# Optimization experiments

Hardware: AMD Instinct MI355X
Metric: run time of the kernel (lower is better)

## Reference

```python
import jax, jax.numpy as jnp
import numpy as np

VOCAB = 50000
D = 300          # w2v vector_size
B = 2048         # sentences
L = 64           # maxlen
S = 2048         # total seeds (= sum of num_clusters[0])
C = 64           # clusters
LS = 8           # maxlen_seed
ANPHA = 0.5


def setup_inputs() -> dict:
    key = jax.random.key(0)
    ks = jax.random.split(key, 4)
    return {
        "sents": jax.random.randint(ks[0], (B, L), 0, VOCAB),
        "seeds": jax.random.randint(ks[1], (S, LS), 0, VOCAB),
        "num_clusters": jnp.full((1, C), S // C, dtype=jnp.int32),
        "num_arr": 0,
        "mask": jnp.ones((B, L), jnp.float32),
        "flag": 1,
        "emb_teacher": jax.random.normal(ks[2], (VOCAB, D), jnp.float32) * 0.1,
        "emb_student": jax.random.normal(ks[3], (VOCAB, D), jnp.float32) * 0.1,
    }


def _sent_emb(tok_emb, mask):
    # masked mean pooling over tokens: tok_emb [B,L,D], mask [B,L]
    denom = jnp.clip(mask.sum(-1, keepdims=True), 1.0)
    return (tok_emb * mask[..., None]).sum(1) / denom


def _seed_emb(tok_emb):
    # plain mean pooling over seed-phrase tokens: [S,LS,D] -> [S,D]
    return tok_emb.mean(1)


def _segment_max_arg(pro, lens):
    # pro [B,S]; lens [C] segment lengths summing to S (ragged segments along axis 1)
    Ssz = pro.shape[1]
    Csz = lens.shape[0]
    csum = jnp.cumsum(lens)
    starts = csum - lens
    seg = jnp.searchsorted(csum, jnp.arange(Ssz), side="right")   # [S] segment ids
    m = jax.ops.segment_max(pro.T, seg, num_segments=Csz)          # [C,B] per-segment max
    is_max = pro.T == m[seg]                                       # [S,B]
    local = jnp.arange(Ssz) - starts[seg]                          # index within segment
    arg = jax.ops.segment_min(jnp.where(is_max, local[:, None], Ssz), seg,
                              num_segments=Csz)                    # first argmax (torch tie rule)
    return m.T, arg.T                                              # [B,C], [B,C]


def _normalize(x):
    # Normalize(): class-probabilities + reliability (confidence vs uniform)
    p = jax.nn.softmax(x, axis=-1)
    reli = jnp.max(p, axis=-1, keepdims=True) - 1.0 / x.shape[-1]
    return p, reli


def reference(sents, seeds, num_clusters, num_arr, mask, flag,
              emb_teacher, emb_student):
    lens = num_clusters[0]

    # teacher branch
    snt_t = _sent_emb(emb_teacher[sents], mask)        # [B,D]
    sd_t = _seed_emb(emb_teacher[seeds])               # [S,D]
    pro_t = jnp.einsum("bd,sd->bs", snt_t, sd_t)       # [B,S]

    # student branch
    snt_s = _sent_emb(emb_student[sents], mask)
    sd_s = _seed_emb(emb_student[seeds])
    pro_s = jnp.einsum("bd,sd->bs", snt_s, sd_s)

    # ragged per-cluster max / argmax (replaces the torch loop + cat)
    pro_s_max, index_max = _segment_max_arg(pro_s, lens)   # [B,C]
    pro_t_max, _ = _segment_max_arg(pro_t, lens)           # [B,C]

    predict_t, reli_t = _normalize(pro_t_max)

    if flag:  # flag is a static python int -> loss branch
        denta = predict_t - pro_s_max
        loss = ((1.0 + ANPHA * jnp.abs(reli_t)) * denta * denta).sum()
        return loss / predict_t.shape[0]
    else:
        return jnp.argmax(pro_s_max, axis=-1)
```

## Files before the change

### kernel.cpp

```cpp
#include <hip/hip_runtime.h>
#include <hip/hip_bf16.h>

#define BB 2048
#define LL 64
#define SS 2048
#define LSEED 8
#define CC 64
#define DD 300
#define KP 320
#define TPAD 48

typedef __attribute__((ext_vector_type(8))) short short8;
typedef __attribute__((ext_vector_type(4))) float f32x4;

__device__ __forceinline__ unsigned enc_f(float f) {
    unsigned u = __float_as_uint(f);
    return (u & 0x80000000u) ? ~u : (u | 0x80000000u);
}
__device__ __forceinline__ float dec_f(unsigned k) {
    unsigned u = (k & 0x80000000u) ? (k ^ 0x80000000u) : ~k;
    return __uint_as_float(u);
}

__global__ void init_kernel(const int* __restrict__ lens,
                            unsigned* __restrict__ keys ,
                            int* __restrict__ seg ) {
    int i = blockIdx.x * 256 + threadIdx.x;
    if (i < 2 * BB * CC) keys[i] = 0u;
    if (i < SS) {
        int c = 0, cum = lens[0];
        while (i >= cum && c < CC - 1) { c++; cum += lens[c]; }
        seg[i] = c;
    }
}

__global__ __launch_bounds__(320) void pool_kernel(
    const int* __restrict__ sents, const int* __restrict__ seeds,
    const float* __restrict__ mask,
    const float* __restrict__ emb_t, const float* __restrict__ emb_s,
    __hip_bfloat16* __restrict__ snt_t, __hip_bfloat16* __restrict__ snt_s,
    __hip_bfloat16* __restrict__ sd_t, __hip_bfloat16* __restrict__ sd_s) {
    int bid = blockIdx.x, tid = threadIdx.x;
    __shared__ int toks[LL];
    __shared__ float msk[LL];
    __shared__ float denom_sh;
    if (bid < BB) {
        int b = bid;
        if (tid < LL) {
            float v = mask[b * LL + tid];
            msk[tid] = v;
            toks[tid] = sents[b * LL + tid];
#pragma unroll
            for (int d = 32; d; d >>= 1) v += __shfl_xor(v, d);
            if (tid == 0) denom_sh = fmaxf(v, 1.0f);
        }
        __syncthreads();
        float at = 0.f, as = 0.f;
        if (tid < DD) {
#pragma unroll 4
            for (int l = 0; l < LL; l++) {
                long o = (long)toks[l] * DD + tid;
                float m = msk[l];
                at = fmaf(m, emb_t[o], at);
                as = fmaf(m, emb_s[o], as);
            }
        }
        float inv = 1.0f / denom_sh;
        float vt = (tid < DD) ? at * inv : 0.f;
        float vs = (tid < DD) ? as * inv : 0.f;
        snt_t[(size_t)b * KP + tid] = __float2bfloat16(vt);
        snt_s[(size_t)b * KP + tid] = __float2bfloat16(vs);
    } else {
        int s = bid - BB;
        if (tid < LSEED) toks[tid] = seeds[s * LSEED + tid];
        __syncthreads();
        float at = 0.f, as = 0.f;
        if (tid < DD) {
#pragma unroll
            for (int l = 0; l < LSEED; l++) {
                long o = (long)toks[l] * DD + tid;
                at += emb_t[o];
                as += emb_s[o];
            }
        }
        float vt = (tid < DD) ? at * (1.0f / LSEED) : 0.f;
        float vs = (tid < DD) ? as * (1.0f / LSEED) : 0.f;
        sd_t[(size_t)s * KP + tid] = __float2bfloat16(vt);
        sd_s[(size_t)s * KP + tid] = __float2bfloat16(vs);
    }
}

__global__ __launch_bounds__(256) void gemm_max_kernel(
    const __hip_bfloat16* __restrict__ snt_t, const __hip_bfloat16* __restrict__ snt_s,
    const __hip_bfloat16* __restrict__ sd_t, const __hip_bfloat16* __restrict__ sd_s,
    const int* __restrict__ seg,
    unsigned* __restrict__ keys_t, unsigned* __restrict__ keys_s) {
    const int branch = blockIdx.z;
    const __hip_bfloat16* Ag = branch ? snt_s : snt_t;
    const __hip_bfloat16* Bg = branch ? sd_s : sd_t;
    unsigned* keys = branch ? keys_s : keys_t;

    const int tid = threadIdx.x;
    const int wave = tid >> 6, lane = tid & 63;
    const int quad = lane >> 4, l16 = lane & 15;
    const int wm = wave >> 1, wn = wave & 1;
    const int row0 = blockIdx.y * 128, col0 = blockIdx.x * 128;

    __shared__ __align__(16) char smem[33792 + 512];
    __hip_bfloat16* As = (__hip_bfloat16*)smem;
    __hip_bfloat16* Bs = As + 128 * TPAD;
    float* Dl = (float*)smem;
    int* segs = (int*)(smem + 33792);

    if (tid < 128) segs[tid] = seg[col0 + tid];

    f32x4 acc[4][4];
#pragma unroll
    for (int i = 0; i < 4; i++)
#pragma unroll
        for (int j = 0; j < 4; j++) acc[i][j] = (f32x4)0.f;

    for (int kt = 0; kt < KP / 32; kt++) {
        const int k0 = kt * 32;
        __syncthreads();
#pragma unroll
        for (int i = 0; i < 2; i++) {
            int c = tid + 256 * i;
            int r = c >> 2, p = c & 3;
            *(float4*)(As + r * TPAD + p * 8) =
                *(const float4*)(Ag + (size_t)(row0 + r) * KP + k0 + p * 8);
            *(float4*)(Bs + r * TPAD + p * 8) =
                *(const float4*)(Bg + (size_t)(col0 + r) * KP + k0 + p * 8);
        }
        __syncthreads();
        short8 af[4], bfr[4];
#pragma unroll
        for (int mt = 0; mt < 4; mt++)
            af[mt] = *(const short8*)(As + (wm * 64 + mt * 16 + l16) * TPAD + quad * 8);
#pragma unroll
        for (int nt = 0; nt < 4; nt++)
            bfr[nt] = *(const short8*)(Bs + (wn * 64 + nt * 16 + l16) * TPAD + quad * 8);
#pragma unroll
        for (int mt = 0; mt < 4; mt++)
#pragma unroll
            for (int nt = 0; nt < 4; nt++)
                acc[mt][nt] = __builtin_amdgcn_mfma_f32_16x16x32_bf16(
                    af[mt], bfr[nt], acc[mt][nt], 0, 0, 0);
    }

#pragma unroll 1
    for (int h = 0; h < 2; h++) {
        __syncthreads();
        if (wn == h) {
#pragma unroll
            for (int mt = 0; mt < 4; mt++)
#pragma unroll
                for (int nt = 0; nt < 4; nt++)
#pragma unroll
                    for (int reg = 0; reg < 4; reg++)
                        Dl[(wm * 64 + mt * 16 + quad * 4 + reg) * 66 + nt * 16 + l16] =
                            acc[mt][nt][reg];
        }
        __syncthreads();
        int r = tid >> 1, j0 = (tid & 1) * 32;
        float cur = Dl[r * 66 + j0];
        int cs = segs[h * 64 + j0];
#pragma unroll
        for (int j = 1; j < 32; j++) {
            int sgj = segs[h * 64 + j0 + j];
            float v = Dl[r * 66 + j0 + j];
            if (sgj == cs) {
                cur = fmaxf(cur, v);
            } else {
                atomicMax(&keys[(size_t)(row0 + r) * CC + cs], enc_f(cur));
                cs = sgj;
                cur = v;
            }
        }
        atomicMax(&keys[(size_t)(row0 + r) * CC + cs], enc_f(cur));
    }
}

__global__ __launch_bounds__(256) void loss_kernel(
    const unsigned* __restrict__ keys_t, const unsigned* __restrict__ keys_s,
    float* __restrict__ partials) {
    int tid = threadIdx.x, w = tid >> 6, lane = tid & 63;
    int row = blockIdx.x * 4 + w;
    float t = dec_f(keys_t[row * CC + lane]);
    float s = dec_f(keys_s[row * CC + lane]);
    float m = t;
#pragma unroll
    for (int d = 32; d; d >>= 1) m = fmaxf(m, __shfl_xor(m, d));
    float e = expf(t - m);
    float sum = e;
#pragma unroll
    for (int d = 32; d; d >>= 1) sum += __shfl_xor(sum, d);
    float p = e / sum;
    float reli = 1.0f / sum - (1.0f / CC);
    float denta = p - s;
    float term = (1.0f + 0.5f * fabsf(reli)) * denta * denta;
#pragma unroll
    for (int d = 32; d; d >>= 1) term += __shfl_xor(term, d);
    __shared__ float blk[4];
    if (lane == 0) blk[w] = term;
    __syncthreads();
    if (tid == 0) partials[blockIdx.x] = blk[0] + blk[1] + blk[2] + blk[3];
}

__global__ void final_kernel(const float* __restrict__ partials, float* __restrict__ out) {
    int tid = threadIdx.x;
    float v = partials[tid] + partials[tid + 256];
#pragma unroll
    for (int d = 32; d; d >>= 1) v += __shfl_xor(v, d);
    __shared__ float blk[4];
    if ((tid & 63) == 0) blk[tid >> 6] = v;
    __syncthreads();
    if (tid == 0) out[0] = (blk[0] + blk[1] + blk[2] + blk[3]) * (1.0f / BB);
}

extern "C" void kernel_launch(void* const* d_in, const int* in_sizes, int n_in,
                              void* d_out, int out_size, void* d_ws, size_t ws_size,
                              hipStream_t stream) {
    const int*   sents = (const int*)d_in[0];
    const int*   seeds = (const int*)d_in[1];
    const int*   lens  = (const int*)d_in[2];
    const float* mask  = (const float*)d_in[4];
    const float* emb_t = (const float*)d_in[6];
    const float* emb_s = (const float*)d_in[7];
    float* out = (float*)d_out;

    char* w = (char*)d_ws;
    __hip_bfloat16* snt_t = (__hip_bfloat16*)w; w += (size_t)BB * KP * 2;
    __hip_bfloat16* snt_s = (__hip_bfloat16*)w; w += (size_t)BB * KP * 2;
    __hip_bfloat16* sd_t  = (__hip_bfloat16*)w; w += (size_t)SS * KP * 2;
    __hip_bfloat16* sd_s  = (__hip_bfloat16*)w; w += (size_t)SS * KP * 2;
    unsigned* keys_t = (unsigned*)w; w += (size_t)BB * CC * 4;
    unsigned* keys_s = (unsigned*)w; w += (size_t)BB * CC * 4;
    int* seg = (int*)w;              w += (size_t)SS * 4;
    float* partials = (float*)w;     w += (size_t)(BB / 4) * 4;

    init_kernel<<<(2 * BB * CC + 255) / 256, 256, 0, stream>>>(lens, keys_t, seg);
    pool_kernel<<<BB + SS, 320, 0, stream>>>(sents, seeds, mask, emb_t, emb_s,
                                             snt_t, snt_s, sd_t, sd_s);
    gemm_max_kernel<<<dim3(SS / 128, BB / 128, 2), 256, 0, stream>>>(
        snt_t, snt_s, sd_t, sd_s, seg, keys_t, keys_s);
    loss_kernel<<<BB / 4, 256, 0, stream>>>(keys_t, keys_s, partials);
    final_kernel<<<1, 256, 0, stream>>>(partials, out);
}
```

Baseline: 198.8 us.

## Fuse init into pooling, vectorize gathers, use direct-to-LDS loads, atomic final sum

Folds the key/segment initialization into the pooling kernel and replaces the final reduction kernel with an atomicAdd in the loss kernel, cutting two launches. Pooling now uses 256 threads that each gather float4 chunks, with three token groups reduced through shared memory. The GEMM tile loads use global_load_lds to write straight into unpadded LDS instead of going through registers, which may add LDS bank conflicts on the fragment reads. Keys are zeroed by pool blocks, which works only because BB+SS blocks times 64 equals 2*BB*CC, and the float atomicAdd makes the final sum order nondeterministic.

```diff
diff --git a/kernel.cpp b/kernel.cpp
--- a/kernel.cpp
+++ b/kernel.cpp
@@ -7,8 +7,8 @@
 #define LSEED 8
 #define CC 64
 #define DD 300
+#define NC4 75
 #define KP 320
-#define TPAD 48
 
 typedef __attribute__((ext_vector_type(8))) short short8;
 typedef __attribute__((ext_vector_type(4))) float f32x4;
@@ -21,31 +21,48 @@
     unsigned u = (k & 0x80000000u) ? (k ^ 0x80000000u) : ~k;
     return __uint_as_float(u);
 }
-
-__global__ void init_kernel(const int* __restrict__ lens,
-                            unsigned* __restrict__ keys ,
-                            int* __restrict__ seg ) {
-    int i = blockIdx.x * 256 + threadIdx.x;
-    if (i < 2 * BB * CC) keys[i] = 0u;
-    if (i < SS) {
-        int c = 0, cum = lens[0];
-        while (i >= cum && c < CC - 1) { c++; cum += lens[c]; }
-        seg[i] = c;
-    }
-}
-
-__global__ __launch_bounds__(320) void pool_kernel(
+__device__ __forceinline__ unsigned short f2bf(float f) {
+    unsigned u = __float_as_uint(f);
+    u += 0x7fffu + ((u >> 16) & 1u);
+    return (unsigned short)(u >> 16);
+}
+__device__ __forceinline__ void gload_lds16(const void* g, void* l) {
+    __builtin_amdgcn_global_load_lds(
+        (const __attribute__((address_space(1))) void*)g,
+        (__attribute__((address_space(3))) void*)l, 16, 0, 0);
+}
+
+__global__ __launch_bounds__(256) void pool_kernel(
     const int* __restrict__ sents, const int* __restrict__ seeds,
-    const float* __restrict__ mask,
+    const int* __restrict__ lens, const float* __restrict__ mask,
     const float* __restrict__ emb_t, const float* __restrict__ emb_s,
-    __hip_bfloat16* __restrict__ snt_t, __hip_bfloat16* __restrict__ snt_s,
-    __hip_bfloat16* __restrict__ sd_t, __hip_bfloat16* __restrict__ sd_s) {
-    int bid = blockIdx.x, tid = threadIdx.x;
+    unsigned short* __restrict__ snt_t, unsigned short* __restrict__ snt_s,
+    unsigned short* __restrict__ sd_t, unsigned short* __restrict__ sd_s,
+    unsigned* __restrict__ keys_all, int* __restrict__ seg,
+    float* __restrict__ out0) {
+    const int bid = blockIdx.x, tid = threadIdx.x;
+
+    if (tid < 64) keys_all[bid * 64 + tid] = 0u;
+    if (bid == 0) {
+        if (tid == 0) *out0 = 0.f;
+        for (int i = tid * 8; i < tid * 8 + 8; i++) {
+            int c = 0, cum = lens[0];
+            while (i >= cum && c < CC - 1) { c++; cum += lens[c]; }
+            seg[i] = c;
+        }
+    }
+
+    __shared__ float4 pt[3 * NC4];
+    __shared__ float4 ps[3 * NC4];
     __shared__ int toks[LL];
     __shared__ float msk[LL];
     __shared__ float denom_sh;
+
+    const int g = tid / NC4;
+    const int c = tid - g * NC4;
+
     if (bid < BB) {
-        int b = bid;
+        const int b = bid;
         if (tid < LL) {
             float v = mask[b * LL + tid];
             msk[tid] = v;
@@ -55,49 +72,86 @@
             if (tid == 0) denom_sh = fmaxf(v, 1.0f);
         }
         __syncthreads();
-        float at = 0.f, as = 0.f;
-        if (tid < DD) {
+        if (g < 3) {
+            float4 at = {0.f, 0.f, 0.f, 0.f}, as = {0.f, 0.f, 0.f, 0.f};
 #pragma unroll 4
-            for (int l = 0; l < LL; l++) {
-                long o = (long)toks[l] * DD + tid;
+            for (int l = g; l < LL; l += 3) {
+                size_t o = (size_t)toks[l] * DD;
                 float m = msk[l];
-                at = fmaf(m, emb_t[o], at);
-                as = fmaf(m, emb_s[o], as);
+                float4 vt = *(const float4*)(emb_t + o + 4 * c);
+                float4 vs = *(const float4*)(emb_s + o + 4 * c);
+                at.x = fmaf(m, vt.x, at.x); at.y = fmaf(m, vt.y, at.y);
+                at.z = fmaf(m, vt.z, at.z); at.w = fmaf(m, vt.w, at.w);
+                as.x = fmaf(m, vs.x, as.x); as.y = fmaf(m, vs.y, as.y);
+                as.z = fmaf(m, vs.z, as.z); as.w = fmaf(m, vs.w, as.w);
             }
-        }
-        float inv = 1.0f / denom_sh;
-        float vt = (tid < DD) ? at * inv : 0.f;
-        float vs = (tid < DD) ? as * inv : 0.f;
-        snt_t[(size_t)b * KP + tid] = __float2bfloat16(vt);
-        snt_s[(size_t)b * KP + tid] = __float2bfloat16(vs);
+            pt[g * NC4 + c] = at;
+            ps[g * NC4 + c] = as;
+        }
+        __syncthreads();
+        float scale = 1.0f / denom_sh;
+        if (tid < 150) {
+            int table = tid / NC4, cc = tid - table * NC4;
+            const float4* P = table ? ps : pt;
+            float4 a = P[cc], b2 = P[NC4 + cc], d2 = P[2 * NC4 + cc];
+            ushort4 o;
+            o.x = f2bf((a.x + b2.x + d2.x) * scale);
+            o.y = f2bf((a.y + b2.y + d2.y) * scale);
+            o.z = f2bf((a.z + b2.z + d2.z) * scale);
+            o.w = f2bf((a.w + b2.w + d2.w) * scale);
+            unsigned short* dst = (table ? snt_s : snt_t) + (size_t)b * KP + 4 * cc;
+            *(ushort4*)dst = o;
+        } else if (tid >= 160 && tid < 170) {
+            int k = tid - 160;
+            unsigned short* dst = ((k < 5) ? snt_t : snt_s) + (size_t)b * KP + 300 + 4 * (k % 5);
+            *(ushort4*)dst = (ushort4){0, 0, 0, 0};
+        }
     } else {
-        int s = bid - BB;
+        const int s = bid - BB;
         if (tid < LSEED) toks[tid] = seeds[s * LSEED + tid];
         __syncthreads();
-        float at = 0.f, as = 0.f;
-        if (tid < DD) {
-#pragma unroll
-            for (int l = 0; l < LSEED; l++) {
-                long o = (long)toks[l] * DD + tid;
-                at += emb_t[o];
-                as += emb_s[o];
+        if (g < 3) {
+            float4 at = {0.f, 0.f, 0.f, 0.f}, as = {0.f, 0.f, 0.f, 0.f};
+#pragma unroll
+            for (int l = g; l < LSEED; l += 3) {
+                size_t o = (size_t)toks[l] * DD;
+                float4 vt = *(const float4*)(emb_t + o + 4 * c);
+                float4 vs = *(const float4*)(emb_s + o + 4 * c);
+                at.x += vt.x; at.y += vt.y; at.z += vt.z; at.w += vt.w;
+                as.x += vs.x; as.y += vs.y; as.z += vs.z; as.w += vs.w;
             }
-        }
-        float vt = (tid < DD) ? at * (1.0f / LSEED) : 0.f;
-        float vs = (tid < DD) ? as * (1.0f / LSEED) : 0.f;
-        sd_t[(size_t)s * KP + tid] = __float2bfloat16(vt);
-        sd_s[(size_t)s * KP + tid] = __float2bfloat16(vs);
+            pt[g * NC4 + c] = at;
+            ps[g * NC4 + c] = as;
+        }
+        __syncthreads();
+        const float scale = 1.0f / LSEED;
+        if (tid < 150) {
+            int table = tid / NC4, cc = tid - table * NC4;
+            const float4* P = table ? ps : pt;
+            float4 a = P[cc], b2 = P[NC4 + cc], d2 = P[2 * NC4 + cc];
+            ushort4 o;
+            o.x = f2bf((a.x + b2.x + d2.x) * scale);
+            o.y = f2bf((a.y + b2.y + d2.y) * scale);
+            o.z = f2bf((a.z + b2.z + d2.z) * scale);
+            o.w = f2bf((a.w + b2.w + d2.w) * scale);
+            unsigned short* dst = (table ? sd_s : sd_t) + (size_t)s * KP + 4 * cc;
+            *(ushort4*)dst = o;
+        } else if (tid >= 160 && tid < 170) {
+            int k = tid - 160;
+            unsigned short* dst = ((k < 5) ? sd_t : sd_s) + (size_t)s * KP + 300 + 4 * (k % 5);
+            *(ushort4*)dst = (ushort4){0, 0, 0, 0};
+        }
     }
 }
 
 __global__ __launch_bounds__(256) void gemm_max_kernel(
-    const __hip_bfloat16* __restrict__ snt_t, const __hip_bfloat16* __restrict__ snt_s,
-    const __hip_bfloat16* __restrict__ sd_t, const __hip_bfloat16* __restrict__ sd_s,
+    const unsigned short* __restrict__ snt_t, const unsigned short* __restrict__ snt_s,
+    const unsigned short* __restrict__ sd_t, const unsigned short* __restrict__ sd_s,
     const int* __restrict__ seg,
     unsigned* __restrict__ keys_t, unsigned* __restrict__ keys_s) {
     const int branch = blockIdx.z;
-    const __hip_bfloat16* Ag = branch ? snt_s : snt_t;
-    const __hip_bfloat16* Bg = branch ? sd_s : sd_t;
+    const unsigned short* Ag = branch ? snt_s : snt_t;
+    const unsigned short* Bg = branch ? sd_s : sd_t;
     unsigned* keys = branch ? keys_s : keys_t;
 
     const int tid = threadIdx.x;
@@ -107,39 +161,41 @@
     const int row0 = blockIdx.y * 128, col0 = blockIdx.x * 128;
 
     __shared__ __align__(16) char smem[33792 + 512];
-    __hip_bfloat16* As = (__hip_bfloat16*)smem;
-    __hip_bfloat16* Bs = As + 128 * TPAD;
+    unsigned short* As = (unsigned short*)smem;
+    unsigned short* Bs = As + 128 * 32;
     float* Dl = (float*)smem;
     int* segs = (int*)(smem + 33792);
 
     if (tid < 128) segs[tid] = seg[col0 + tid];
 
+    const int lr = lane >> 2, lp = lane & 3;
+
     f32x4 acc[4][4];
 #pragma unroll
     for (int i = 0; i < 4; i++)
 #pragma unroll
         for (int j = 0; j < 4; j++) acc[i][j] = (f32x4)0.f;
 
+#pragma unroll 1
     for (int kt = 0; kt < KP / 32; kt++) {
         const int k0 = kt * 32;
         __syncthreads();
 #pragma unroll
         for (int i = 0; i < 2; i++) {
-            int c = tid + 256 * i;
-            int r = c >> 2, p = c & 3;
-            *(float4*)(As + r * TPAD + p * 8) =
-                *(const float4*)(Ag + (size_t)(row0 + r) * KP + k0 + p * 8);
-            *(float4*)(Bs + r * TPAD + p * 8) =
-                *(const float4*)(Bg + (size_t)(col0 + r) * KP + k0 + p * 8);
+            int rb = wave * 32 + i * 16;
+            gload_lds16(Ag + (size_t)(row0 + rb + lr) * KP + k0 + lp * 8,
+                        As + rb * 32);
+            gload_lds16(Bg + (size_t)(col0 + rb + lr) * KP + k0 + lp * 8,
+                        Bs + rb * 32);
         }
         __syncthreads();
         short8 af[4], bfr[4];
 #pragma unroll
         for (int mt = 0; mt < 4; mt++)
-            af[mt] = *(const short8*)(As + (wm * 64 + mt * 16 + l16) * TPAD + quad * 8);
+            af[mt] = *(const short8*)(As + (wm * 64 + mt * 16 + l16) * 32 + quad * 8);
 #pragma unroll
         for (int nt = 0; nt < 4; nt++)
-            bfr[nt] = *(const short8*)(Bs + (wn * 64 + nt * 16 + l16) * TPAD + quad * 8);
+            bfr[nt] = *(const short8*)(Bs + (wn * 64 + nt * 16 + l16) * 32 + quad * 8);
 #pragma unroll
         for (int mt = 0; mt < 4; mt++)
 #pragma unroll
@@ -183,7 +239,7 @@
 
 __global__ __launch_bounds__(256) void loss_kernel(
     const unsigned* __restrict__ keys_t, const unsigned* __restrict__ keys_s,
-    float* __restrict__ partials) {
+    float* __restrict__ out) {
     int tid = threadIdx.x, w = tid >> 6, lane = tid & 63;
     int row = blockIdx.x * 4 + w;
     float t = dec_f(keys_t[row * CC + lane]);
@@ -204,18 +260,8 @@
     __shared__ float blk[4];
     if (lane == 0) blk[w] = term;
     __syncthreads();
-    if (tid == 0) partials[blockIdx.x] = blk[0] + blk[1] + blk[2] + blk[3];
-}
-
-__global__ void final_kernel(const float* __restrict__ partials, float* __restrict__ out) {
-    int tid = threadIdx.x;
-    float v = partials[tid] + partials[tid + 256];
-#pragma unroll
-    for (int d = 32; d; d >>= 1) v += __shfl_xor(v, d);
-    __shared__ float blk[4];
-    if ((tid & 63) == 0) blk[tid >> 6] = v;
-    __syncthreads();
-    if (tid == 0) out[0] = (blk[0] + blk[1] + blk[2] + blk[3]) * (1.0f / BB);
+    if (tid == 0)
+        atomicAdd(out, (blk[0] + blk[1] + blk[2] + blk[3]) * (1.0f / BB));
 }
 
 extern "C" void kernel_launch(void* const* d_in, const int* in_sizes, int n_in,
@@ -230,20 +276,18 @@
     float* out = (float*)d_out;
 
     char* w = (char*)d_ws;
-    __hip_bfloat16* snt_t = (__hip_bfloat16*)w; w += (size_t)BB * KP * 2;
-    __hip_bfloat16* snt_s = (__hip_bfloat16*)w; w += (size_t)BB * KP * 2;
-    __hip_bfloat16* sd_t  = (__hip_bfloat16*)w; w += (size_t)SS * KP * 2;
-    __hip_bfloat16* sd_s  = (__hip_bfloat16*)w; w += (size_t)SS * KP * 2;
+    unsigned short* snt_t = (unsigned short*)w; w += (size_t)BB * KP * 2;
+    unsigned short* snt_s = (unsigned short*)w; w += (size_t)BB * KP * 2;
+    unsigned short* sd_t  = (unsigned short*)w; w += (size_t)SS * KP * 2;
+    unsigned short* sd_s  = (unsigned short*)w; w += (size_t)SS * KP * 2;
     unsigned* keys_t = (unsigned*)w; w += (size_t)BB * CC * 4;
     unsigned* keys_s = (unsigned*)w; w += (size_t)BB * CC * 4;
     int* seg = (int*)w;              w += (size_t)SS * 4;
-    float* partials = (float*)w;     w += (size_t)(BB / 4) * 4;
-
-    init_kernel<<<(2 * BB * CC + 255) / 256, 256, 0, stream>>>(lens, keys_t, seg);
-    pool_kernel<<<BB + SS, 320, 0, stream>>>(sents, seeds, mask, emb_t, emb_s,
-                                             snt_t, snt_s, sd_t, sd_s);
+
+    pool_kernel<<<BB + SS, 256, 0, stream>>>(sents, seeds, lens, mask, emb_t, emb_s,
+                                             snt_t, snt_s, sd_t, sd_s,
+                                             keys_t, seg, out);
     gemm_max_kernel<<<dim3(SS / 128, BB / 128, 2), 256, 0, stream>>>(
         snt_t, snt_s, sd_t, sd_s, seg, keys_t, keys_s);
-    loss_kernel<<<BB / 4, 256, 0, stream>>>(keys_t, keys_s, partials);
-    final_kernel<<<1, 256, 0, stream>>>(partials, out);
-}
+    loss_kernel<<<BB / 4, 256, 0, stream>>>(keys_t, keys_s, out);
+}
```

New measurement: 197.4 us (median of 2 runs). About the same (-0.7%).
